# Kernel tuning notes

Measured on AMD Instinct MI355X. Metric: run time of the kernel, lower is better.

## Reference

```python
import jax, jax.numpy as jnp
import numpy as np

T, D, E, K = 16384, 2048, 128, 8

def setup_inputs() -> dict:
    key = jax.random.key(0)
    k1, k2 = jax.random.split(key)
    hidden_states = jax.random.normal(k1, (T, D), dtype=jnp.float32)
    weight = jax.random.normal(k2, (E, D), dtype=jnp.float32) * 0.02
    return {"hidden_states": hidden_states, "weight": weight}

def reference(hidden_states, weight):
    # (T, D) @ (D, E) -> (T, E) router logits
    x = hidden_states.reshape(-1, weight.shape[1])
    logits = jnp.einsum('td,ed->te', x, weight)
    # softmax in float32 over experts
    router_logits = jax.nn.softmax(logits.astype(jnp.float32), axis=-1)
    # top-k selection + renormalization so selected weights sum to 1
    router_weights, router_indices = jax.lax.top_k(router_logits, K)
    router_weights = router_weights / jnp.sum(router_weights, axis=-1, keepdims=True)
    return (router_logits, router_weights, router_indices)
```

## Files before the change

### kernel.cpp

```cpp
#include <hip/hip_runtime.h>
#include <math.h>


constexpr int T = 16384;
constexpr int D = 2048;
constexpr int E = 128;
constexpr int K = 8;

constexpr int BM = 32;
constexpr int BK = 32;
constexpr int NS = 5;

typedef int i32x4  __attribute__((ext_vector_type(4)));
typedef int i32x16 __attribute__((ext_vector_type(16)));

__device__ __forceinline__ void slice5(float x, float c, float ic, int out[NS]) {
    float r = x;
#pragma unroll
    for (int s = 0; s < NS; ++s) {
        float q = rintf(r * c);
        out[s] = (int)q;
        r = fmaf(q, -ic, r);
        c *= 128.f;
        ic *= (1.f / 128.f);
    }
}

__global__ __launch_bounds__(256)
void w_slice(const float* __restrict__ W, signed char* __restrict__ Ws)
{
    const int e  = blockIdx.x;
    const int k0 = threadIdx.x * 8;
    const float* src = W + (size_t)e * D + k0;
    float4 v0 = *(const float4*)(src);
    float4 v1 = *(const float4*)(src + 4);
    const float x[8] = {v0.x, v0.y, v0.z, v0.w, v1.x, v1.y, v1.z, v1.w};
    int b[8][NS];
#pragma unroll
    for (int t = 0; t < 8; ++t) slice5(x[t], 512.f, 1.f / 512.f, b[t]);
#pragma unroll
    for (int s = 0; s < NS; ++s) {
        unsigned lo = (unsigned)(b[0][s] & 255)        | ((unsigned)(b[1][s] & 255) << 8) |
                      ((unsigned)(b[2][s] & 255) << 16) | ((unsigned)(b[3][s] & 255) << 24);
        unsigned hi = (unsigned)(b[4][s] & 255)        | ((unsigned)(b[5][s] & 255) << 8) |
                      ((unsigned)(b[6][s] & 255) << 16) | ((unsigned)(b[7][s] & 255) << 24);
        *(int2*)(Ws + (size_t)s * E * D + (size_t)e * D + k0) = make_int2((int)lo, (int)hi);
    }
}

__global__ __launch_bounds__(256, 2)
void router_fused(const float* __restrict__ X,
                  const signed char* __restrict__ Ws,
                  float* __restrict__ out)
{
    __shared__ __align__(16) signed char As[NS][2][BM][16];
    __shared__ double Ld[BM][E];

    const int tid = threadIdx.x;
    const long t0 = (long)blockIdx.x * BM;

    const int ar = tid >> 3;
    const int ac = (tid & 7) << 2;
    const float* Xp = X + (t0 + ar) * (long)D + ac;

    const int l  = tid & 63;
    const int wv = tid >> 6;
    const int mr = l & 31;
    const int mh = l >> 5;

    const size_t wbase = (size_t)(wv * 32 + mr) * D + (size_t)mh * 16;
    const i32x4* wp0 = (const i32x4*)(Ws + 0UL * E * D + wbase);
    const i32x4* wp1 = (const i32x4*)(Ws + 1UL * E * D + wbase);
    const i32x4* wp2 = (const i32x4*)(Ws + 2UL * E * D + wbase);
    const i32x4* wp3 = (const i32x4*)(Ws + 3UL * E * D + wbase);
    const i32x4* wp4 = (const i32x4*)(Ws + 4UL * E * D + wbase);

    i32x16 acc0 = {}, acc1 = {}, acc2 = {}, acc3 = {}, acc4 = {};

    float4 xv = *(const float4*)(Xp);

    for (int k0 = 0; k0 < D; k0 += BK) {
        const int ki = k0 >> 4;

        i32x4 b0 = wp0[ki];
        i32x4 b1 = wp1[ki];
        i32x4 b2 = wp2[ki];
        i32x4 b3 = wp3[ki];
        i32x4 b4 = wp4[ki];

        int bx0[NS], bx1[NS], bx2[NS], bx3[NS];
        slice5(xv.x, 16.f, 1.f / 16.f, bx0);
        slice5(xv.y, 16.f, 1.f / 16.f, bx1);
        slice5(xv.z, 16.f, 1.f / 16.f, bx2);
        slice5(xv.w, 16.f, 1.f / 16.f, bx3);

        __syncthreads();
        {
            char* dst = (char*)&As[0][ac >> 4][ar][ac & 15];
#pragma unroll
            for (int s = 0; s < NS; ++s) {
                unsigned pk = (unsigned)(bx0[s] & 255)        | ((unsigned)(bx1[s] & 255) << 8) |
                              ((unsigned)(bx2[s] & 255) << 16) | ((unsigned)(bx3[s] & 255) << 24);
                *(int*)(dst + s * 1024) = (int)pk;
            }
        }
        __syncthreads();

        const int kn = k0 + BK;
        if (kn < D) xv = *(const float4*)(Xp + kn);

        i32x4 a0 = *(const i32x4*)&As[0][mh][mr][0];
        i32x4 a1 = *(const i32x4*)&As[1][mh][mr][0];
        i32x4 a2 = *(const i32x4*)&As[2][mh][mr][0];
        i32x4 a3 = *(const i32x4*)&As[3][mh][mr][0];
        i32x4 a4 = *(const i32x4*)&As[4][mh][mr][0];

        acc0 = __builtin_amdgcn_mfma_i32_32x32x32_i8(a0, b0, acc0, 0, 0, 0);
        acc1 = __builtin_amdgcn_mfma_i32_32x32x32_i8(a0, b1, acc1, 0, 0, 0);
        acc1 = __builtin_amdgcn_mfma_i32_32x32x32_i8(a1, b0, acc1, 0, 0, 0);
        acc2 = __builtin_amdgcn_mfma_i32_32x32x32_i8(a0, b2, acc2, 0, 0, 0);
        acc2 = __builtin_amdgcn_mfma_i32_32x32x32_i8(a1, b1, acc2, 0, 0, 0);
        acc2 = __builtin_amdgcn_mfma_i32_32x32x32_i8(a2, b0, acc2, 0, 0, 0);
        acc3 = __builtin_amdgcn_mfma_i32_32x32x32_i8(a0, b3, acc3, 0, 0, 0);
        acc3 = __builtin_amdgcn_mfma_i32_32x32x32_i8(a1, b2, acc3, 0, 0, 0);
        acc3 = __builtin_amdgcn_mfma_i32_32x32x32_i8(a2, b1, acc3, 0, 0, 0);
        acc3 = __builtin_amdgcn_mfma_i32_32x32x32_i8(a3, b0, acc3, 0, 0, 0);
        acc4 = __builtin_amdgcn_mfma_i32_32x32x32_i8(a0, b4, acc4, 0, 0, 0);
        acc4 = __builtin_amdgcn_mfma_i32_32x32x32_i8(a1, b3, acc4, 0, 0, 0);
        acc4 = __builtin_amdgcn_mfma_i32_32x32x32_i8(a2, b2, acc4, 0, 0, 0);
        acc4 = __builtin_amdgcn_mfma_i32_32x32x32_i8(a3, b1, acc4, 0, 0, 0);
        acc4 = __builtin_amdgcn_mfma_i32_32x32x32_i8(a4, b0, acc4, 0, 0, 0);
    }

#pragma unroll
    for (int r = 0; r < 16; ++r) {
        const int row = (r & 3) + 8 * (r >> 2) + 4 * mh;
        const double lg = (double)acc0[r] * 0x1p-13
                        + (double)acc1[r] * 0x1p-20
                        + (double)acc2[r] * 0x1p-27
                        + (double)acc3[r] * 0x1p-34
                        + (double)acc4[r] * 0x1p-41;
        Ld[row][wv * 32 + mr] = lg;
    }
    __syncthreads();

    float* outL  = out;
    float* outWt = out + (long)T * E;
    float* outId = outWt + (long)T * K;
    const int tx = tid & 15;

    for (int rep = 0; rep < 2; ++rep) {
        const int tt = (tid >> 4) + rep * 16;
        const long t = t0 + tt;

        double acc[8];
#pragma unroll
        for (int j = 0; j < 8; ++j) acc[j] = Ld[tt][(tx << 3) + j];

        double m = acc[0];
#pragma unroll
        for (int j = 1; j < 8; ++j) m = fmax(m, acc[j]);
#pragma unroll
        for (int mask = 1; mask <= 8; mask <<= 1)
            m = fmax(m, __shfl_xor(m, mask, 64));

        float e[8]; float s = 0.f;
#pragma unroll
        for (int j = 0; j < 8; ++j) { e[j] = __expf((float)(acc[j] - m)); s += e[j]; }
#pragma unroll
        for (int mask = 1; mask <= 8; mask <<= 1)
            s += __shfl_xor(s, mask, 64);
        const float inv = 1.f / s;

        float4 st0 = {e[0] * inv, e[1] * inv, e[2] * inv, e[3] * inv};
        float4 st1 = {e[4] * inv, e[5] * inv, e[6] * inv, e[7] * inv};
        *(float4*)&outL[t * E + (tx << 3)]     = st0;
        *(float4*)&outL[t * E + (tx << 3) + 4] = st1;

        double v[8];
#pragma unroll
        for (int j = 0; j < 8; ++j) v[j] = acc[j];

        float pk[K]; int ik[K]; float tsum = 0.f;
#pragma unroll
        for (int r = 0; r < K; ++r) {
            double bv = -1.0e300; int bi = 0x7fffffff;
#pragma unroll
            for (int j = 0; j < 8; ++j) {
                const int idx = (tx << 3) + j;
                const bool better = (v[j] > bv) || (v[j] == bv && idx < bi);
                bv = better ? v[j] : bv;
                bi = better ? idx : bi;
            }
#pragma unroll
            for (int mask = 1; mask <= 8; mask <<= 1) {
                const double ov = __shfl_xor(bv, mask, 64);
                const int    oi = __shfl_xor(bi, mask, 64);
                const bool better = (ov > bv) || (ov == bv && oi < bi);
                bv = better ? ov : bv;
                bi = better ? oi : bi;
            }
            const float pw = __expf((float)(bv - m)) * inv;
            pk[r] = pw; ik[r] = bi; tsum += pw;
            const bool own  = ((bi >> 3) == tx);
            const int  slot = bi & 7;
#pragma unroll
            for (int j = 0; j < 8; ++j)
                v[j] = (own && j == slot) ? -1.0e300 : v[j];
        }

        if (tx == 0) {
            const float rinv = 1.f / tsum;
#pragma unroll
            for (int r = 0; r < K; ++r) {
                outWt[t * K + r] = pk[r] * rinv;
                outId[t * K + r] = (float)ik[r];
            }
        }
    }
}

extern "C" void kernel_launch(void* const* d_in, const int* in_sizes, int n_in,
                              void* d_out, int out_size, void* d_ws, size_t ws_size,
                              hipStream_t stream)
{
    const float* X = (const float*)d_in[0];
    const float* W = (const float*)d_in[1];
    float* out = (float*)d_out;
    signed char* Ws = (signed char*)d_ws;

    w_slice<<<dim3(E), dim3(256), 0, stream>>>(W, Ws);
    router_fused<<<dim3(T / BM), dim3(256), 0, stream>>>(X, Ws, out);
}
```

Baseline: 290.4 us.

## Double-buffer A slices in shared memory and process two K-chunks per barrier

The main loop now stages the next 64-wide K step of X slices into a second shared-memory buffer while the MFMAs consume the current one. This cuts barriers from two per 32-wide step to one per 64-wide step and prefetches X two chunks ahead. The weight-slicing kernel is also split over twice as many blocks, each handling four floats per thread. The cost is more shared memory (about 20 KB for the A buffers) and more live registers, which may reduce occupancy under the two-blocks-per-CU launch bound.

```diff
diff --git a/kernel.cpp b/kernel.cpp
--- a/kernel.cpp
+++ b/kernel.cpp
@@ -7,9 +7,9 @@
 constexpr int E = 128;
 constexpr int K = 8;
 
-constexpr int BM = 32;
-constexpr int BK = 32;
-constexpr int NS = 5;
+constexpr int BM  = 32;
+constexpr int NS  = 5;
+constexpr int NP  = D / 64;
 
 typedef int i32x4  __attribute__((ext_vector_type(4)));
 typedef int i32x16 __attribute__((ext_vector_type(16)));
@@ -29,22 +29,19 @@
 __global__ __launch_bounds__(256)
 void w_slice(const float* __restrict__ W, signed char* __restrict__ Ws)
 {
-    const int e  = blockIdx.x;
-    const int k0 = threadIdx.x * 8;
-    const float* src = W + (size_t)e * D + k0;
-    float4 v0 = *(const float4*)(src);
-    float4 v1 = *(const float4*)(src + 4);
-    const float x[8] = {v0.x, v0.y, v0.z, v0.w, v1.x, v1.y, v1.z, v1.w};
-    int b[8][NS];
-#pragma unroll
-    for (int t = 0; t < 8; ++t) slice5(x[t], 512.f, 1.f / 512.f, b[t]);
+    const int e  = blockIdx.x >> 1;
+    const int k0 = ((blockIdx.x & 1) << 10) | (threadIdx.x << 2);
+    float4 v = *(const float4*)(W + (size_t)e * D + k0);
+    int b0[NS], b1[NS], b2[NS], b3[NS];
+    slice5(v.x, 512.f, 1.f / 512.f, b0);
+    slice5(v.y, 512.f, 1.f / 512.f, b1);
+    slice5(v.z, 512.f, 1.f / 512.f, b2);
+    slice5(v.w, 512.f, 1.f / 512.f, b3);
 #pragma unroll
     for (int s = 0; s < NS; ++s) {
-        unsigned lo = (unsigned)(b[0][s] & 255)        | ((unsigned)(b[1][s] & 255) << 8) |
-                      ((unsigned)(b[2][s] & 255) << 16) | ((unsigned)(b[3][s] & 255) << 24);
-        unsigned hi = (unsigned)(b[4][s] & 255)        | ((unsigned)(b[5][s] & 255) << 8) |
-                      ((unsigned)(b[6][s] & 255) << 16) | ((unsigned)(b[7][s] & 255) << 24);
-        *(int2*)(Ws + (size_t)s * E * D + (size_t)e * D + k0) = make_int2((int)lo, (int)hi);
+        unsigned pk = (unsigned)(b0[s] & 255)        | ((unsigned)(b1[s] & 255) << 8) |
+                      ((unsigned)(b2[s] & 255) << 16) | ((unsigned)(b3[s] & 255) << 24);
+        *(int*)(Ws + (size_t)s * E * D + (size_t)e * D + k0) = (int)pk;
     }
 }
 
@@ -53,7 +50,7 @@
                   const signed char* __restrict__ Ws,
                   float* __restrict__ out)
 {
-    __shared__ __align__(16) signed char As[NS][2][BM][16];
+    __shared__ __align__(16) signed char As[2][2][NS][2][BM][16];
     __shared__ double Ld[BM][E];
 
     const int tid = threadIdx.x;
@@ -77,44 +74,29 @@
 
     i32x16 acc0 = {}, acc1 = {}, acc2 = {}, acc3 = {}, acc4 = {};
 
-    float4 xv = *(const float4*)(Xp);
-
-    for (int k0 = 0; k0 < D; k0 += BK) {
-        const int ki = k0 >> 4;
-
-        i32x4 b0 = wp0[ki];
-        i32x4 b1 = wp1[ki];
-        i32x4 b2 = wp2[ki];
-        i32x4 b3 = wp3[ki];
-        i32x4 b4 = wp4[ki];
-
+    auto stageChunk = [&](const float4& v, int buf, int chn) {
         int bx0[NS], bx1[NS], bx2[NS], bx3[NS];
-        slice5(xv.x, 16.f, 1.f / 16.f, bx0);
-        slice5(xv.y, 16.f, 1.f / 16.f, bx1);
-        slice5(xv.z, 16.f, 1.f / 16.f, bx2);
-        slice5(xv.w, 16.f, 1.f / 16.f, bx3);
-
-        __syncthreads();
-        {
-            char* dst = (char*)&As[0][ac >> 4][ar][ac & 15];
-#pragma unroll
-            for (int s = 0; s < NS; ++s) {
-                unsigned pk = (unsigned)(bx0[s] & 255)        | ((unsigned)(bx1[s] & 255) << 8) |
-                              ((unsigned)(bx2[s] & 255) << 16) | ((unsigned)(bx3[s] & 255) << 24);
-                *(int*)(dst + s * 1024) = (int)pk;
-            }
-        }
-        __syncthreads();
-
-        const int kn = k0 + BK;
-        if (kn < D) xv = *(const float4*)(Xp + kn);
-
-        i32x4 a0 = *(const i32x4*)&As[0][mh][mr][0];
-        i32x4 a1 = *(const i32x4*)&As[1][mh][mr][0];
-        i32x4 a2 = *(const i32x4*)&As[2][mh][mr][0];
-        i32x4 a3 = *(const i32x4*)&As[3][mh][mr][0];
-        i32x4 a4 = *(const i32x4*)&As[4][mh][mr][0];
-
+        slice5(v.x, 16.f, 1.f / 16.f, bx0);
+        slice5(v.y, 16.f, 1.f / 16.f, bx1);
+        slice5(v.z, 16.f, 1.f / 16.f, bx2);
+        slice5(v.w, 16.f, 1.f / 16.f, bx3);
+        char* dst = (char*)&As[buf][chn][0][ac >> 4][ar][ac & 15];
+#pragma unroll
+        for (int s = 0; s < NS; ++s) {
+            unsigned pk = (unsigned)(bx0[s] & 255)        | ((unsigned)(bx1[s] & 255) << 8) |
+                          ((unsigned)(bx2[s] & 255) << 16) | ((unsigned)(bx3[s] & 255) << 24);
+            *(int*)(dst + s * 1024) = (int)pk;
+        }
+    };
+
+    auto mstep = [&](int buf, int chn,
+                     const i32x4& b0, const i32x4& b1, const i32x4& b2,
+                     const i32x4& b3, const i32x4& b4) {
+        i32x4 a0 = *(const i32x4*)&As[buf][chn][0][mh][mr][0];
+        i32x4 a1 = *(const i32x4*)&As[buf][chn][1][mh][mr][0];
+        i32x4 a2 = *(const i32x4*)&As[buf][chn][2][mh][mr][0];
+        i32x4 a3 = *(const i32x4*)&As[buf][chn][3][mh][mr][0];
+        i32x4 a4 = *(const i32x4*)&As[buf][chn][4][mh][mr][0];
         acc0 = __builtin_amdgcn_mfma_i32_32x32x32_i8(a0, b0, acc0, 0, 0, 0);
         acc1 = __builtin_amdgcn_mfma_i32_32x32x32_i8(a0, b1, acc1, 0, 0, 0);
         acc1 = __builtin_amdgcn_mfma_i32_32x32x32_i8(a1, b0, acc1, 0, 0, 0);
@@ -130,6 +112,37 @@
         acc4 = __builtin_amdgcn_mfma_i32_32x32x32_i8(a2, b2, acc4, 0, 0, 0);
         acc4 = __builtin_amdgcn_mfma_i32_32x32x32_i8(a3, b1, acc4, 0, 0, 0);
         acc4 = __builtin_amdgcn_mfma_i32_32x32x32_i8(a4, b0, acc4, 0, 0, 0);
+    };
+
+    float4 xs0 = *(const float4*)(Xp);
+    float4 xs1 = *(const float4*)(Xp + 32);
+    stageChunk(xs0, 0, 0);
+    stageChunk(xs1, 0, 1);
+    xs0 = *(const float4*)(Xp + 64);
+    xs1 = *(const float4*)(Xp + 96);
+    __syncthreads();
+
+    for (int p = 0; p < NP; ++p) {
+        const int cur = p & 1;
+
+        i32x4 b0 = wp0[4 * p],     b1 = wp1[4 * p],     b2 = wp2[4 * p],
+              b3 = wp3[4 * p],     b4 = wp4[4 * p];
+        i32x4 c0 = wp0[4 * p + 2], c1 = wp1[4 * p + 2], c2 = wp2[4 * p + 2],
+              c3 = wp3[4 * p + 2], c4 = wp4[4 * p + 2];
+
+        if (p < NP - 1) {
+            stageChunk(xs0, cur ^ 1, 0);
+            stageChunk(xs1, cur ^ 1, 1);
+        }
+        if (p < NP - 2) {
+            xs0 = *(const float4*)(Xp + (2 * p + 4) * 32);
+            xs1 = *(const float4*)(Xp + (2 * p + 5) * 32);
+        }
+
+        mstep(cur, 0, b0, b1, b2, b3, b4);
+        mstep(cur, 1, c0, c1, c2, c3, c4);
+
+        __syncthreads();
     }
 
 #pragma unroll
@@ -229,6 +242,6 @@
     float* out = (float*)d_out;
     signed char* Ws = (signed char*)d_ws;
 
-    w_slice<<<dim3(E), dim3(256), 0, stream>>>(W, Ws);
+    w_slice<<<dim3(E * 2), dim3(256), 0, stream>>>(W, Ws);
     router_fused<<<dim3(T / BM), dim3(256), 0, stream>>>(X, Ws, out);
 }
```

After: 277.2 us. -4.6%, faster.
